# Performance work log

Measured on AMD Instinct MI355X. Metric: run time of the kernel, lower is better.

## Reference

```python
import jax, jax.numpy as jnp
import numpy as np

B = 1024
N_NODES = 30
E_PER = 82
IN_F = 128
HID = 256
HEADS = (3, 2, 1)
N_EH = 41


def _lin(k, fi, fo):
    s = 1.0 / np.sqrt(fi)
    kw, kb = jax.random.split(k)
    W = jax.random.uniform(kw, (fi, fo), jnp.float32, -s, s)
    b = jax.random.uniform(kb, (fo,), jnp.float32, -s, s)
    return W, b


def setup_inputs() -> dict:
    key = jax.random.key(0)
    ks = list(jax.random.split(key, 32))
    rng = np.random.default_rng(0)
    # base 30-node graph with E_PER directed edges, no self-loops
    src = rng.integers(0, N_NODES, E_PER)
    dst = (src + rng.integers(1, N_NODES, E_PER)) % N_NODES
    base = np.stack([src, dst])  # [2, E_PER]
    offs = (np.arange(B) * N_NODES)[None, None, :]  # [1,1,B]
    ei = (base[:, :, None] + offs).transpose(0, 2, 1).reshape(2, -1)  # [2, B*E_PER]
    e_h = rng.choice(E_PER, N_EH, replace=False)
    d = {}
    d["x"] = jax.random.normal(ks[0], (B * N_NODES, IN_F), jnp.float32)
    d["edge_index"] = jnp.asarray(ei, dtype=jnp.int32)
    d["e_h_pairs"] = jnp.asarray(base[:, e_h].T, dtype=jnp.int32)  # [N_EH, 2]
    d["Wp"], d["bp"] = _lin(ks[1], IN_F, HID)
    i = 2
    for l, H in enumerate(HEADS):
        d[f"ln_g{l}"] = jnp.ones((HID,), jnp.float32)
        d[f"ln_b{l}"] = jnp.zeros((HID,), jnp.float32)
        d[f"Wl{l}"], d[f"bl{l}"] = _lin(ks[i], HID, H * HID); i += 1
        d[f"Wr{l}"], d[f"br{l}"] = _lin(ks[i], HID, H * HID); i += 1
        d[f"att{l}"] = jax.random.normal(ks[i], (H, HID), jnp.float32) * 0.1; i += 1
        d[f"bias{l}"] = jnp.zeros((HID,), jnp.float32)
    dims = [2 * HID, 256, 128, 128, 1]
    for j in range(4):
        d[f"Wm{j}"], d[f"bm{j}"] = _lin(ks[i], dims[j], dims[j + 1]); i += 1
    return d


def _layer_norm(h, g, b):
    mu = jnp.mean(h, -1, keepdims=True)
    var = jnp.mean((h - mu) ** 2, -1, keepdims=True)
    return (h - mu) * jax.lax.rsqrt(var + 1e-5) * g + b


def _gatv2(h, src, dst, n, Wl, bl, Wr, br, att, bias):
    # PyG GATv2Conv, concat=False (mean over heads), self-loops already in src/dst
    H, C = att.shape
    xl = (h @ Wl + bl).reshape(-1, H, C)  # source transform
    xr = (h @ Wr + br).reshape(-1, H, C)  # target transform
    xj = xl[src]                          # [E,H,C]
    e = jax.nn.leaky_relu(xj + xr[dst], 0.2)
    logits = jnp.einsum('ehc,hc->eh', e, att)  # [E,H]
    m = jax.lax.stop_gradient(jax.ops.segment_max(logits, dst, num_segments=n))
    ex = jnp.exp(logits - m[dst])
    denom = jax.ops.segment_sum(ex, dst, num_segments=n)
    alpha = ex / denom[dst]               # softmax over incoming edges of dst
    out = jax.ops.segment_sum(xj * alpha[..., None], dst, num_segments=n)  # [N,H,C]
    return jnp.mean(out, 1) + bias


def reference(x, edge_index, e_h_pairs, Wp, bp,
              ln_g0, ln_b0, Wl0, bl0, Wr0, br0, att0, bias0,
              ln_g1, ln_b1, Wl1, bl1, Wr1, br1, att1, bias1,
              ln_g2, ln_b2, Wl2, bl2, Wr2, br2, att2, bias2,
              Wm0, bm0, Wm1, bm1, Wm2, bm2, Wm3, bm3):
    n = x.shape[0]
    loops = jnp.arange(n, dtype=edge_index.dtype)
    src = jnp.concatenate([edge_index[0], loops])
    dst = jnp.concatenate([edge_index[1], loops])
    lrelu = lambda v: jax.nn.leaky_relu(v, 0.01)
    h = x @ Wp + bp
    layers = [(ln_g0, ln_b0, Wl0, bl0, Wr0, br0, att0, bias0),
              (ln_g1, ln_b1, Wl1, bl1, Wr1, br1, att1, bias1),
              (ln_g2, ln_b2, Wl2, bl2, Wr2, br2, att2, bias2)]
    for (g, b, Wl, bl, Wr, br, att, bias) in layers:
        hn = _layer_norm(h, g, b)
        hc = _gatv2(hn, src, dst, n, Wl, bl, Wr, br, att, bias)
        h = lrelu(hc) + h  # dropout is identity in eval
    hb = h.reshape(-1, N_NODES, HID)  # [B, 30, 256]
    ef = jnp.concatenate([hb[:, e_h_pairs[:, 0], :], hb[:, e_h_pairs[:, 1], :]], -1)
    o = ef.reshape(-1, 2 * HID)
    o = lrelu(o @ Wm0 + bm0)
    o = lrelu(o @ Wm1 + bm1)
    o = lrelu(o @ Wm2 + bm2)
    o = o @ Wm3 + bm3
    return o.reshape(-1)
```

## Files before the change

### kernel.cpp

```cpp
#include <hip/hip_runtime.h>
#include <hip/hip_bf16.h>
#include <math.h>

#define N_NODES 30
#define E_BASE  82
#define E_TOT   112
#define B_GRAPH 1024
#define HID     256
#define NTOT    (B_GRAPH * N_NODES)
#define MAXIN   32
#define N_EH    41
#define M_MLP   (B_GRAPH * N_EH)

#define META_SRC  0
#define META_DST  E_TOT
#define META_CNT  (2 * E_TOT)
#define META_LIST 256
#define META_INTS 1216

typedef __attribute__((ext_vector_type(8))) short bf16x8;
typedef __attribute__((ext_vector_type(4))) short bf16x4;
typedef __attribute__((ext_vector_type(4))) float f32x4;
#define AS3 __attribute__((address_space(3)))
#define AS1 __attribute__((address_space(1)))

__device__ __forceinline__ void gload_lds16(const void* g, void* l) {
  __builtin_amdgcn_global_load_lds((const AS1 void*)g, (AS3 void*)l, 16, 0, 0);
}

__device__ __forceinline__ float b2f(short s) {
  union { unsigned u; float f; } x;
  x.u = ((unsigned)(unsigned short)s) << 16;
  return x.f;
}

__global__ void build_graph(const int* __restrict__ ei, int* __restrict__ meta) {
  __shared__ int cnt[N_NODES];
  int tid = threadIdx.x;
  if (tid < N_NODES) cnt[tid] = 0;
  __syncthreads();
  if (tid < E_TOT) {
    int s, d;
    if (tid < E_BASE) { s = ei[tid]; d = ei[B_GRAPH * E_BASE + tid]; }
    else              { s = tid - E_BASE; d = s; }
    meta[META_SRC + tid] = s;
    meta[META_DST + tid] = d;
    int pos = atomicAdd(&cnt[d], 1);
    if (pos < MAXIN) meta[META_LIST + d * MAXIN + pos] = tid;
  }
  __syncthreads();
  if (tid < N_NODES) meta[META_CNT + tid] = cnt[tid];
}

struct WtJob { const float* in; int K, N, tstart, ooff; };
struct WtArgs { WtJob j[10]; };

__global__ __launch_bounds__(256)
void transpose_weights(WtArgs args, __hip_bfloat16* __restrict__ out) {
  int b = blockIdx.x;
  int ji = 0;
  #pragma unroll
  for (int i = 1; i < 10; i++) if (b >= args.j[i].tstart) ji = i;
  WtJob jb = args.j[ji];
  int t = b - jb.tstart;
  int ntn = jb.N >> 5;
  int tk = t / ntn, tn = t - tk * ntn;
  int k0 = tk * 32, n0 = tn * 32;
  __shared__ float s[32][33];
  int tx = threadIdx.x & 31, ty = threadIdx.x >> 5;
  #pragma unroll
  for (int p = 0; p < 4; p++)
    s[ty + p * 8][tx] = jb.in[(size_t)(k0 + ty + p * 8) * jb.N + n0 + tx];
  __syncthreads();
  __hip_bfloat16* o = out + jb.ooff;
  #pragma unroll
  for (int p = 0; p < 4; p++) {
    int n = ty + p * 8;
    o[(size_t)(n0 + n) * jb.K + k0 + tx] = __float2bfloat16(s[tx][n]);
  }
}

__global__ __launch_bounds__(256)
void cast_bf16(const float* __restrict__ in, __hip_bfloat16* __restrict__ out, int n8) {
  int i = blockIdx.x * 256 + threadIdx.x;
  if (i >= n8) return;
  float4 v0 = ((const float4*)in)[i * 2];
  float4 v1 = ((const float4*)in)[i * 2 + 1];
  __hip_bfloat16 t[8];
  t[0] = __float2bfloat16(v0.x); t[1] = __float2bfloat16(v0.y);
  t[2] = __float2bfloat16(v0.z); t[3] = __float2bfloat16(v0.w);
  t[4] = __float2bfloat16(v1.x); t[5] = __float2bfloat16(v1.y);
  t[6] = __float2bfloat16(v1.z); t[7] = __float2bfloat16(v1.w);
  *(bf16x8*)&out[(size_t)i * 8] = *(bf16x8*)t;
}

template<int ACT, int OUTBF>
__global__ __launch_bounds__(256)
void gemm_mfma(const __hip_bfloat16* __restrict__ A, const __hip_bfloat16* __restrict__ Bt,
               const float* __restrict__ bias, const float* __restrict__ bias2,
               void* __restrict__ Cv, int M, int K, int N, int N1)
{
  __shared__ __hip_bfloat16 sA[128 * 32];
  __shared__ __hip_bfloat16 sB[128 * 32];
  const int tid = threadIdx.x;
  const int lane = tid & 63;
  const int wave = tid >> 6;
  const int wx = wave & 1, wy = wave >> 1;
  const int bm = blockIdx.x, bn = blockIdx.y;
  const int mrow = lane & 15, quad = lane >> 4;

  const int r0 = tid >> 2, kc0 = (tid & 3) * 8;
  const __hip_bfloat16* Ag0 = A + (size_t)(bm * 128 + r0) * K + kc0;
  const __hip_bfloat16* Ag1 = A + (size_t)(bm * 128 + r0 + 64) * K + kc0;
  const __hip_bfloat16* Bg0 = Bt + (size_t)(bn * 128 + r0) * K + kc0;
  const __hip_bfloat16* Bg1 = Bt + (size_t)(bn * 128 + r0 + 64) * K + kc0;

  f32x4 acc[4][4];
  #pragma unroll
  for (int i = 0; i < 4; i++)
    #pragma unroll
    for (int j = 0; j < 4; j++)
      acc[i][j] = (f32x4){0.f, 0.f, 0.f, 0.f};

  for (int kt = 0; kt < K; kt += 32) {
    __syncthreads();
    gload_lds16(Ag0 + kt, &sA[tid * 8]);
    gload_lds16(Ag1 + kt, &sA[2048 + tid * 8]);
    gload_lds16(Bg0 + kt, &sB[tid * 8]);
    gload_lds16(Bg1 + kt, &sB[2048 + tid * 8]);
    __syncthreads();

    bf16x8 af[4], bfr[4];
    #pragma unroll
    for (int i = 0; i < 4; i++) {
      af[i]  = *(const bf16x8*)&sA[(wy * 64 + i * 16 + mrow) * 32 + quad * 8];
      bfr[i] = *(const bf16x8*)&sB[(wx * 64 + i * 16 + mrow) * 32 + quad * 8];
    }
    #pragma unroll
    for (int i = 0; i < 4; i++)
      #pragma unroll
      for (int j = 0; j < 4; j++)
        acc[i][j] = __builtin_amdgcn_mfma_f32_16x16x32_bf16(af[i], bfr[j], acc[i][j], 0, 0, 0);
  }

  #pragma unroll
  for (int i = 0; i < 4; i++) {
    #pragma unroll
    for (int r = 0; r < 4; r++) {
      size_t row = (size_t)bm * 128 + wy * 64 + i * 16 + quad * 4 + r;
      #pragma unroll
      for (int j = 0; j < 4; j++) {
        int col = bn * 128 + wx * 64 + j * 16 + mrow;
        float bc = (col < N1) ? bias[col] : bias2[col - N1];
        float v = acc[i][j][r] + bc;
        if (ACT) v = v > 0.f ? v : 0.01f * v;
        if (OUTBF) ((__hip_bfloat16*)Cv)[row * N + col] = __float2bfloat16(v);
        else       ((float*)Cv)[row * N + col] = v;
      }
    }
  }
}

__global__ __launch_bounds__(256)
void gemm_mfma_pair(const float* __restrict__ h, const int* __restrict__ pairs,
                    const __hip_bfloat16* __restrict__ Bt, const float* __restrict__ bias,
                    __hip_bfloat16* __restrict__ C, int N)
{
  const int K = 512;
  __shared__ __hip_bfloat16 sA[128 * 32];
  __shared__ __hip_bfloat16 sB[128 * 32];
  const int tid = threadIdx.x;
  const int lane = tid & 63;
  const int wave = tid >> 6;
  const int wx = wave & 1, wy = wave >> 1;
  const int bm = blockIdx.x, bn = blockIdx.y;
  const int mrow = lane & 15, quad = lane >> 4;

  const float* pu[2]; const float* pv[2]; int sub[2];
  #pragma unroll
  for (int cI = 0; cI < 2; cI++) {
    int c = tid + cI * 256;
    int r0 = c >> 2; sub[cI] = (c & 3) * 8;
    int R = bm * 128 + r0;
    int b = R / N_EH, p = R - b * N_EH;
    int u = pairs[p * 2], v = pairs[p * 2 + 1];
    pu[cI] = h + ((size_t)b * N_NODES + u) * HID;
    pv[cI] = h + ((size_t)b * N_NODES + v) * HID;
  }

  const int r0 = tid >> 2, kc0 = (tid & 3) * 8;
  const __hip_bfloat16* Bg0 = Bt + (size_t)(bn * 128 + r0) * K + kc0;
  const __hip_bfloat16* Bg1 = Bt + (size_t)(bn * 128 + r0 + 64) * K + kc0;

  f32x4 acc[4][4];
  #pragma unroll
  for (int i = 0; i < 4; i++)
    #pragma unroll
    for (int j = 0; j < 4; j++)
      acc[i][j] = (f32x4){0.f, 0.f, 0.f, 0.f};

  for (int kt = 0; kt < K; kt += 32) {
    float4 av[2][2];
    #pragma unroll
    for (int cI = 0; cI < 2; cI++) {
      const float* src = (kt < 256 ? pu[cI] + kt : pv[cI] + kt - 256) + sub[cI];
      av[cI][0] = *(const float4*)src;
      av[cI][1] = *(const float4*)(src + 4);
    }
    __syncthreads();
    #pragma unroll
    for (int cI = 0; cI < 2; cI++) {
      __hip_bfloat16 t[8];
      t[0] = __float2bfloat16(av[cI][0].x); t[1] = __float2bfloat16(av[cI][0].y);
      t[2] = __float2bfloat16(av[cI][0].z); t[3] = __float2bfloat16(av[cI][0].w);
      t[4] = __float2bfloat16(av[cI][1].x); t[5] = __float2bfloat16(av[cI][1].y);
      t[6] = __float2bfloat16(av[cI][1].z); t[7] = __float2bfloat16(av[cI][1].w);
      *(bf16x8*)&sA[(tid + cI * 256) * 8] = *(bf16x8*)t;
    }
    gload_lds16(Bg0 + kt, &sB[tid * 8]);
    gload_lds16(Bg1 + kt, &sB[2048 + tid * 8]);
    __syncthreads();

    bf16x8 af[4], bfr[4];
    #pragma unroll
    for (int i = 0; i < 4; i++) {
      af[i]  = *(const bf16x8*)&sA[(wy * 64 + i * 16 + mrow) * 32 + quad * 8];
      bfr[i] = *(const bf16x8*)&sB[(wx * 64 + i * 16 + mrow) * 32 + quad * 8];
    }
    #pragma unroll
    for (int i = 0; i < 4; i++)
      #pragma unroll
      for (int j = 0; j < 4; j++)
        acc[i][j] = __builtin_amdgcn_mfma_f32_16x16x32_bf16(af[i], bfr[j], acc[i][j], 0, 0, 0);
  }

  #pragma unroll
  for (int i = 0; i < 4; i++) {
    #pragma unroll
    for (int r = 0; r < 4; r++) {
      size_t row = (size_t)bm * 128 + wy * 64 + i * 16 + quad * 4 + r;
      #pragma unroll
      for (int j = 0; j < 4; j++) {
        int col = bn * 128 + wx * 64 + j * 16 + mrow;
        float v = acc[i][j][r] + bias[col];
        v = v > 0.f ? v : 0.01f * v;
        C[row * N + col] = __float2bfloat16(v);
      }
    }
  }
}

__global__ __launch_bounds__(256)
void layernorm(const float* __restrict__ h, const float* __restrict__ g,
               const float* __restrict__ b, __hip_bfloat16* __restrict__ hn)
{
  const int wv = threadIdx.x >> 6, lane = threadIdx.x & 63;
  const size_t row = (size_t)blockIdx.x * 4 + wv;
  const float* hr = h + row * HID;
  float v[4];
  float sum = 0.f;
  #pragma unroll
  for (int j = 0; j < 4; j++) { v[j] = hr[lane + 64 * j]; sum += v[j]; }
  #pragma unroll
  for (int off = 32; off; off >>= 1) sum += __shfl_xor(sum, off);
  float mu = sum * (1.f / 256.f);
  float vs = 0.f;
  #pragma unroll
  for (int j = 0; j < 4; j++) { float d = v[j] - mu; vs += d * d; }
  #pragma unroll
  for (int off = 32; off; off >>= 1) vs += __shfl_xor(vs, off);
  float rs = rsqrtf(vs * (1.f / 256.f) + 1e-5f);
  __hip_bfloat16* outr = hn + row * HID;
  #pragma unroll
  for (int j = 0; j < 4; j++) {
    int c = lane + 64 * j;
    outr[c] = __float2bfloat16((v[j] - mu) * rs * g[c] + b[c]);
  }
}

__global__ __launch_bounds__(256)
void gat_alpha(const __hip_bfloat16* __restrict__ xcat,
               const float* __restrict__ att, float* __restrict__ alphaG,
               const int* __restrict__ meta, int H)
{
  __shared__ float slog[E_TOT];
  __shared__ float smax[N_NODES];
  __shared__ float sden[N_NODES];
  __shared__ int ssrc[E_TOT], sdst[E_TOT], scnt[N_NODES], slist[N_NODES * MAXIN];

  const int tid = threadIdx.x;
  const int g = blockIdx.x, hh = blockIdx.y;
  const size_t nodebase = (size_t)g * N_NODES;
  const int S = 2 * H * HID;

  if (tid < E_TOT) { ssrc[tid] = meta[META_SRC + tid]; sdst[tid] = meta[META_DST + tid]; }
  if (tid < N_NODES) { scnt[tid] = meta[META_CNT + tid]; sden[tid] = 0.f; }
  for (int i = tid; i < N_NODES * MAXIN; i += 256) slist[i] = meta[META_LIST + i];

  const int wv = tid >> 6, l32 = tid & 31, esub = (tid >> 5) & 1;
  const int c0 = l32 * 8;
  float attr[8];
  #pragma unroll
  for (int j = 0; j < 8; j++) attr[j] = att[hh * HID + c0 + j];
  __syncthreads();

  #pragma unroll
  for (int pass = 0; pass < 14; pass++) {
    int e = pass * 8 + wv * 2 + esub;
    int s = ssrc[e], d = sdst[e];
    bf16x8 a = *(const bf16x8*)&xcat[(nodebase + s) * S + hh * HID + c0];
    bf16x8 b = *(const bf16x8*)&xcat[(nodebase + d) * S + (H + hh) * HID + c0];
    float sum = 0.f;
    #pragma unroll
    for (int j = 0; j < 8; j++) {
      float v = b2f(a[j]) + b2f(b[j]);
      v = v > 0.f ? v : 0.2f * v;
      sum += v * attr[j];
    }
    #pragma unroll
    for (int off = 16; off; off >>= 1) sum += __shfl_xor(sum, off);
    if (l32 == 0) slog[e] = sum;
  }
  __syncthreads();

  if (tid < N_NODES) {
    int cnt = scnt[tid];
    const int* lst = &slist[tid * MAXIN];
    float m = -1e30f;
    for (int i = 0; i < cnt; i++) m = fmaxf(m, slog[lst[i]]);
    smax[tid] = m;
  }
  __syncthreads();
  if (tid < E_TOT) {
    float ex = expf(slog[tid] - smax[sdst[tid]]);
    slog[tid] = ex;
    atomicAdd(&sden[sdst[tid]], ex);
  }
  __syncthreads();
  if (tid < E_TOT)
    alphaG[((size_t)g * H + hh) * E_TOT + tid] = slog[tid] / sden[sdst[tid]];
}

template<int DO_LN>
__global__ __launch_bounds__(256, 4)
void gat_agg(const __hip_bfloat16* __restrict__ xcat, const float* __restrict__ alphaG,
             const float* __restrict__ bias, float* __restrict__ h,
             const float* __restrict__ lnG, const float* __restrict__ lnB,
             __hip_bfloat16* __restrict__ hn, const int* __restrict__ meta, int H)
{
  __shared__ __hip_bfloat16 sxl[2][N_NODES * HID];
  __shared__ float salpha[2][E_TOT];
  __shared__ int ssrc[E_TOT], scnt[N_NODES], slist[N_NODES * MAXIN];

  const int tid = threadIdx.x;
  const int g = blockIdx.x;
  const size_t nodebase = (size_t)g * N_NODES;
  const int S = 2 * H * HID;
  const int c4 = tid & 63;
  const int ng = tid >> 6;

  if (tid < E_TOT) ssrc[tid] = meta[META_SRC + tid];
  if (tid < N_NODES) scnt[tid] = meta[META_CNT + tid];
  for (int i = tid; i < N_NODES * MAXIN; i += 256) slist[i] = meta[META_LIST + i];

  float4 hres[8];
  #pragma unroll
  for (int ki = 0; ki < 8; ki++) {
    int k = ng + ki * 4;
    if (k < N_NODES) hres[ki] = *(const float4*)&h[(nodebase + k) * HID + c4 * 4];
  }

  {
    int i = tid;
    #pragma unroll
    for (int p = 0; p < 4; p++, i += 256) {
      if (i < N_NODES * HID / 8) {
        int node = i >> 5, c = (i & 31) * 8;
        gload_lds16(&xcat[(nodebase + node) * S + 0 * HID + c], &sxl[0][(size_t)i * 8]);
      }
    }
    if (tid < E_TOT) salpha[0][tid] = alphaG[((size_t)g * H + 0) * E_TOT + tid];
  }

  float acc[8][4];
  #pragma unroll
  for (int ki = 0; ki < 8; ki++)
    #pragma unroll
    for (int j = 0; j < 4; j++) acc[ki][j] = 0.f;

  for (int hh = 0; hh < H; hh++) {
    const int buf = hh & 1;
    __syncthreads();
    if (hh + 1 < H) {
      const int nb = buf ^ 1;
      int i = tid;
      #pragma unroll
      for (int p = 0; p < 4; p++, i += 256) {
        if (i < N_NODES * HID / 8) {
          int node = i >> 5, c = (i & 31) * 8;
          gload_lds16(&xcat[(nodebase + node) * S + (hh + 1) * HID + c], &sxl[nb][(size_t)i * 8]);
        }
      }
      if (tid < E_TOT) salpha[nb][tid] = alphaG[((size_t)g * H + hh + 1) * E_TOT + tid];
    }
    #pragma unroll
    for (int ki = 0; ki < 8; ki++) {
      int k = ng + ki * 4;
      if (k < N_NODES) {
        int cnt = scnt[k];
        const int* lst = &slist[k * MAXIN];
        for (int i = 0; i < cnt; i++) {
          int e = lst[i];
          float al = salpha[buf][e];
          bf16x4 v = *(const bf16x4*)&sxl[buf][ssrc[e] * HID + c4 * 4];
          acc[ki][0] += al * b2f(v[0]);
          acc[ki][1] += al * b2f(v[1]);
          acc[ki][2] += al * b2f(v[2]);
          acc[ki][3] += al * b2f(v[3]);
        }
      }
    }
  }

  const float invH = 1.f / (float)H;
  const float4 bs = *(const float4*)&bias[c4 * 4];
  float4 gv, bv;
  if (DO_LN) {
    gv = *(const float4*)&lnG[c4 * 4];
    bv = *(const float4*)&lnB[c4 * 4];
  }
  #pragma unroll
  for (int ki = 0; ki < 8; ki++) {
    int k = ng + ki * 4;
    if (k < N_NODES) {
      float o0 = acc[ki][0] * invH + bs.x; o0 = o0 > 0.f ? o0 : 0.01f * o0; o0 += hres[ki].x;
      float o1 = acc[ki][1] * invH + bs.y; o1 = o1 > 0.f ? o1 : 0.01f * o1; o1 += hres[ki].y;
      float o2 = acc[ki][2] * invH + bs.z; o2 = o2 > 0.f ? o2 : 0.01f * o2; o2 += hres[ki].z;
      float o3 = acc[ki][3] * invH + bs.w; o3 = o3 > 0.f ? o3 : 0.01f * o3; o3 += hres[ki].w;
      float4 o4 = {o0, o1, o2, o3};
      *(float4*)&h[(nodebase + k) * HID + c4 * 4] = o4;
      if (DO_LN) {
        float sum = o0 + o1 + o2 + o3;
        #pragma unroll
        for (int off = 32; off; off >>= 1) sum += __shfl_xor(sum, off);
        float mu = sum * (1.f / 256.f);
        float d0 = o0 - mu, d1 = o1 - mu, d2 = o2 - mu, d3 = o3 - mu;
        float vs = d0 * d0 + d1 * d1 + d2 * d2 + d3 * d3;
        #pragma unroll
        for (int off = 32; off; off >>= 1) vs += __shfl_xor(vs, off);
        float rs = rsqrtf(vs * (1.f / 256.f) + 1e-5f);
        __hip_bfloat16 t[4];
        t[0] = __float2bfloat16(d0 * rs * gv.x + bv.x);
        t[1] = __float2bfloat16(d1 * rs * gv.y + bv.y);
        t[2] = __float2bfloat16(d2 * rs * gv.z + bv.z);
        t[3] = __float2bfloat16(d3 * rs * gv.w + bv.w);
        *(bf16x4*)&hn[(nodebase + k) * HID + c4 * 4] = *(bf16x4*)t;
      }
    }
  }
}

__global__ __launch_bounds__(256)
void mlp_out(const float* __restrict__ o3, const float* __restrict__ w,
             const float* __restrict__ b3, float* __restrict__ out)
{
  const int wv = threadIdx.x >> 6, lane = threadIdx.x & 63;
  const int row = blockIdx.x * 4 + wv;
  const float* orow = o3 + (size_t)row * 128;
  float s = orow[lane] * w[lane] + orow[lane + 64] * w[lane + 64];
  #pragma unroll
  for (int off = 32; off; off >>= 1) s += __shfl_xor(s, off);
  if (lane == 0) out[row] = s + b3[0];
}

extern "C" void kernel_launch(void* const* d_in, const int* in_sizes, int n_in,
                              void* d_out, int out_size, void* d_ws, size_t ws_size,
                              hipStream_t stream) {
  const float* x     = (const float*)d_in[0];
  const int*   ei    = (const int*)d_in[1];
  const int*   pairs = (const int*)d_in[2];
  const float* bp    = (const float*)d_in[4];
  const float *lng[3], *lnb[3], *bl[3], *br[3], *att[3], *bias[3];
  const float *WlF[3], *WrF[3];
  for (int l = 0; l < 3; l++) {
    int base = 5 + l * 8;
    lng[l]  = (const float*)d_in[base + 0];
    lnb[l]  = (const float*)d_in[base + 1];
    WlF[l]  = (const float*)d_in[base + 2];
    bl[l]   = (const float*)d_in[base + 3];
    WrF[l]  = (const float*)d_in[base + 4];
    br[l]   = (const float*)d_in[base + 5];
    att[l]  = (const float*)d_in[base + 6];
    bias[l] = (const float*)d_in[base + 7];
  }
  const float* WmF[4] = {(const float*)d_in[29], (const float*)d_in[31],
                         (const float*)d_in[33], (const float*)d_in[35]};
  const float* bm[4] = {(const float*)d_in[30], (const float*)d_in[32],
                        (const float*)d_in[34], (const float*)d_in[36]};

  float* ws  = (float*)d_ws;
  float* h   = ws;
  __hip_bfloat16* hnb = (__hip_bfloat16*)(ws + 7864320);
  __hip_bfloat16* xb  = (__hip_bfloat16*)(ws + 9830400);
  __hip_bfloat16* xcat = (__hip_bfloat16*)(ws + 11796480);
  float* alphaG = ws + 35389440;
  __hip_bfloat16* wbuf = (__hip_bfloat16*)(ws + 35733504);
  int*   meta = (int*)(ws + 36233216);
  __hip_bfloat16* o1b = (__hip_bfloat16*)xcat;
  __hip_bfloat16* o2b = (__hip_bfloat16*)(ws + 17170432);
  float* o3 = ws + 23592960;
  float* out = (float*)d_out;

  const int oWp = 0, oWl0 = 32768, oWr0 = 229376, oWl1 = 425984, oWr1 = 557056;
  const int oWl2 = 688128, oWr2 = 753664, oWm0 = 819200, oWm1 = 950272, oWm2 = 983040;

  build_graph<<<1, 128, 0, stream>>>(ei, meta);

  WtArgs wa;
  wa.j[0] = {(const float*)d_in[3], 128, 256,   0, oWp };
  wa.j[1] = {WlF[0],              256, 768,  32, oWl0};
  wa.j[2] = {WrF[0],              256, 768, 224, oWr0};
  wa.j[3] = {WlF[1],              256, 512, 416, oWl1};
  wa.j[4] = {WrF[1],              256, 512, 544, oWr1};
  wa.j[5] = {WlF[2],              256, 256, 672, oWl2};
  wa.j[6] = {WrF[2],              256, 256, 736, oWr2};
  wa.j[7] = {WmF[0],              512, 256, 800, oWm0};
  wa.j[8] = {WmF[1],              256, 128, 928, oWm1};
  wa.j[9] = {WmF[2],              128, 128, 960, oWm2};
  transpose_weights<<<976, 256, 0, stream>>>(wa, wbuf);

  cast_bf16<<<1920, 256, 0, stream>>>(x, xb, NTOT * 128 / 8);

  gemm_mfma<0, 0><<<dim3(NTOT / 128, 2), 256, 0, stream>>>(xb, wbuf + oWp, bp, bp, h,
                                                           NTOT, 128, 256, 256);

  layernorm<<<NTOT / 4, 256, 0, stream>>>(h, lng[0], lnb[0], hnb);

  const int Hs[3] = {3, 2, 1};
  const int oWl[3] = {oWl0, oWl1, oWl2};
  for (int l = 0; l < 3; l++) {
    int N = 2 * Hs[l] * HID;
    gemm_mfma<0, 1><<<dim3(NTOT / 128, N / 128), 256, 0, stream>>>(
        hnb, wbuf + oWl[l], bl[l], br[l], xcat, NTOT, HID, N, N / 2);
    gat_alpha<<<dim3(B_GRAPH, Hs[l]), 256, 0, stream>>>(xcat, att[l], alphaG, meta, Hs[l]);
    if (l < 2)
      gat_agg<1><<<B_GRAPH, 256, 0, stream>>>(xcat, alphaG, bias[l], h,
                                              lng[l + 1], lnb[l + 1], hnb, meta, Hs[l]);
    else
      gat_agg<0><<<B_GRAPH, 256, 0, stream>>>(xcat, alphaG, bias[l], h,
                                              nullptr, nullptr, nullptr, meta, Hs[l]);
  }

  gemm_mfma_pair<<<dim3(M_MLP / 128, 2), 256, 0, stream>>>(h, pairs, wbuf + oWm0, bm[0], o1b, 256);
  gemm_mfma<1, 1><<<dim3(M_MLP / 128, 1), 256, 0, stream>>>(o1b, wbuf + oWm1, bm[1], bm[1], o2b,
                                                            M_MLP, 256, 128, 128);
  gemm_mfma<1, 0><<<dim3(M_MLP / 128, 1), 256, 0, stream>>>(o2b, wbuf + oWm2, bm[2], bm[2], o3,
                                                            M_MLP, 128, 128, 128);
  mlp_out<<<M_MLP / 4, 256, 0, stream>>>(o3, WmF[3], bm[3], out);
}
```

Baseline: 462.8 us.

## Fuse input bf16 cast into first GEMM and vectorize GEMM epilogue stores

Removes the separate cast_bf16 kernel by adding a GEMM variant that loads fp32 activations directly and converts them to bf16 while staging into LDS. It also swaps the MFMA operand order so each lane holds four consecutive output columns, which lets the epilogue issue 4-wide vector stores and vector bias loads instead of scalar ones. This saves one kernel launch and a full round trip of the bf16 copy of x through memory. The cost is that the fp32 A loads now go through registers rather than direct-to-LDS loads.

```diff
diff --git a/kernel.cpp b/kernel.cpp
--- a/kernel.cpp
+++ b/kernel.cpp
@@ -80,18 +80,26 @@
   }
 }
 
-__global__ __launch_bounds__(256)
-void cast_bf16(const float* __restrict__ in, __hip_bfloat16* __restrict__ out, int n8) {
-  int i = blockIdx.x * 256 + threadIdx.x;
-  if (i >= n8) return;
-  float4 v0 = ((const float4*)in)[i * 2];
-  float4 v1 = ((const float4*)in)[i * 2 + 1];
-  __hip_bfloat16 t[8];
-  t[0] = __float2bfloat16(v0.x); t[1] = __float2bfloat16(v0.y);
-  t[2] = __float2bfloat16(v0.z); t[3] = __float2bfloat16(v0.w);
-  t[4] = __float2bfloat16(v1.x); t[5] = __float2bfloat16(v1.y);
-  t[6] = __float2bfloat16(v1.z); t[7] = __float2bfloat16(v1.w);
-  *(bf16x8*)&out[(size_t)i * 8] = *(bf16x8*)t;
+template<int ACT, int OUTBF>
+__device__ __forceinline__ void store4(void* Cv, size_t row, int colbase, int N,
+                                       const f32x4 a, const float* bias,
+                                       const float* bias2, int N1) {
+  const float* bp = (colbase < N1) ? bias + colbase : bias2 + (colbase - N1);
+  float4 bv = *(const float4*)bp;
+  float v0 = a[0] + bv.x, v1 = a[1] + bv.y, v2 = a[2] + bv.z, v3 = a[3] + bv.w;
+  if (ACT) {
+    v0 = v0 > 0.f ? v0 : 0.01f * v0; v1 = v1 > 0.f ? v1 : 0.01f * v1;
+    v2 = v2 > 0.f ? v2 : 0.01f * v2; v3 = v3 > 0.f ? v3 : 0.01f * v3;
+  }
+  if (OUTBF) {
+    union { __hip_bfloat16 t[4]; uint2 u; } P;
+    P.t[0] = __float2bfloat16(v0); P.t[1] = __float2bfloat16(v1);
+    P.t[2] = __float2bfloat16(v2); P.t[3] = __float2bfloat16(v3);
+    *(uint2*)&((__hip_bfloat16*)Cv)[row * N + colbase] = P.u;
+  } else {
+    float4 o = {v0, v1, v2, v3};
+    *(float4*)&((float*)Cv)[row * N + colbase] = o;
+  }
 }
 
 template<int ACT, int OUTBF>
@@ -140,23 +148,91 @@
     for (int i = 0; i < 4; i++)
       #pragma unroll
       for (int j = 0; j < 4; j++)
-        acc[i][j] = __builtin_amdgcn_mfma_f32_16x16x32_bf16(af[i], bfr[j], acc[i][j], 0, 0, 0);
+        acc[i][j] = __builtin_amdgcn_mfma_f32_16x16x32_bf16(bfr[j], af[i], acc[i][j], 0, 0, 0);
   }
 
   #pragma unroll
   for (int i = 0; i < 4; i++) {
-    #pragma unroll
-    for (int r = 0; r < 4; r++) {
-      size_t row = (size_t)bm * 128 + wy * 64 + i * 16 + quad * 4 + r;
+    size_t row = (size_t)bm * 128 + wy * 64 + i * 16 + mrow;
+    #pragma unroll
+    for (int j = 0; j < 4; j++) {
+      int colbase = bn * 128 + wx * 64 + j * 16 + quad * 4;
+      store4<ACT, OUTBF>(Cv, row, colbase, N, acc[i][j], bias, bias2, N1);
+    }
+  }
+}
+
+template<int ACT, int OUTBF>
+__global__ __launch_bounds__(256)
+void gemm_mfma_f32a(const float* __restrict__ A, const __hip_bfloat16* __restrict__ Bt,
+                    const float* __restrict__ bias, void* __restrict__ Cv,
+                    int M, int K, int N)
+{
+  __shared__ __hip_bfloat16 sA[128 * 32];
+  __shared__ __hip_bfloat16 sB[128 * 32];
+  const int tid = threadIdx.x;
+  const int lane = tid & 63;
+  const int wave = tid >> 6;
+  const int wx = wave & 1, wy = wave >> 1;
+  const int bm = blockIdx.x, bn = blockIdx.y;
+  const int mrow = lane & 15, quad = lane >> 4;
+
+  const int r0 = tid >> 2, kc0 = (tid & 3) * 8;
+  const float* Ag0 = A + (size_t)(bm * 128 + r0) * K + kc0;
+  const float* Ag1 = A + (size_t)(bm * 128 + r0 + 64) * K + kc0;
+  const __hip_bfloat16* Bg0 = Bt + (size_t)(bn * 128 + r0) * K + kc0;
+  const __hip_bfloat16* Bg1 = Bt + (size_t)(bn * 128 + r0 + 64) * K + kc0;
+
+  f32x4 acc[4][4];
+  #pragma unroll
+  for (int i = 0; i < 4; i++)
+    #pragma unroll
+    for (int j = 0; j < 4; j++)
+      acc[i][j] = (f32x4){0.f, 0.f, 0.f, 0.f};
+
+  for (int kt = 0; kt < K; kt += 32) {
+    float4 a00 = *(const float4*)(Ag0 + kt);
+    float4 a01 = *(const float4*)(Ag0 + kt + 4);
+    float4 a10 = *(const float4*)(Ag1 + kt);
+    float4 a11 = *(const float4*)(Ag1 + kt + 4);
+    __syncthreads();
+    {
+      __hip_bfloat16 t[8];
+      t[0] = __float2bfloat16(a00.x); t[1] = __float2bfloat16(a00.y);
+      t[2] = __float2bfloat16(a00.z); t[3] = __float2bfloat16(a00.w);
+      t[4] = __float2bfloat16(a01.x); t[5] = __float2bfloat16(a01.y);
+      t[6] = __float2bfloat16(a01.z); t[7] = __float2bfloat16(a01.w);
+      *(bf16x8*)&sA[tid * 8] = *(bf16x8*)t;
+      t[0] = __float2bfloat16(a10.x); t[1] = __float2bfloat16(a10.y);
+      t[2] = __float2bfloat16(a10.z); t[3] = __float2bfloat16(a10.w);
+      t[4] = __float2bfloat16(a11.x); t[5] = __float2bfloat16(a11.y);
+      t[6] = __float2bfloat16(a11.z); t[7] = __float2bfloat16(a11.w);
+      *(bf16x8*)&sA[2048 + tid * 8] = *(bf16x8*)t;
+    }
+    gload_lds16(Bg0 + kt, &sB[tid * 8]);
+    gload_lds16(Bg1 + kt, &sB[2048 + tid * 8]);
+    __syncthreads();
+
+    bf16x8 af[4], bfr[4];
+    #pragma unroll
+    for (int i = 0; i < 4; i++) {
+      af[i]  = *(const bf16x8*)&sA[(wy * 64 + i * 16 + mrow) * 32 + quad * 8];
+      bfr[i] = *(const bf16x8*)&sB[(wx * 64 + i * 16 + mrow) * 32 + quad * 8];
+    }
+    #pragma unroll
+    for (int i = 0; i < 4; i++)
       #pragma unroll
-      for (int j = 0; j < 4; j++) {
-        int col = bn * 128 + wx * 64 + j * 16 + mrow;
-        float bc = (col < N1) ? bias[col] : bias2[col - N1];
-        float v = acc[i][j][r] + bc;
-        if (ACT) v = v > 0.f ? v : 0.01f * v;
-        if (OUTBF) ((__hip_bfloat16*)Cv)[row * N + col] = __float2bfloat16(v);
-        else       ((float*)Cv)[row * N + col] = v;
-      }
+      for (int j = 0; j < 4; j++)
+        acc[i][j] = __builtin_amdgcn_mfma_f32_16x16x32_bf16(bfr[j], af[i], acc[i][j], 0, 0, 0);
+  }
+
+  #pragma unroll
+  for (int i = 0; i < 4; i++) {
+    size_t row = (size_t)bm * 128 + wy * 64 + i * 16 + mrow;
+    #pragma unroll
+    for (int j = 0; j < 4; j++) {
+      int colbase = bn * 128 + wx * 64 + j * 16 + quad * 4;
+      store4<ACT, OUTBF>(Cv, row, colbase, N, acc[i][j], bias, bias, N);
     }
   }
 }
@@ -231,21 +307,16 @@
     for (int i = 0; i < 4; i++)
       #pragma unroll
       for (int j = 0; j < 4; j++)
-        acc[i][j] = __builtin_amdgcn_mfma_f32_16x16x32_bf16(af[i], bfr[j], acc[i][j], 0, 0, 0);
+        acc[i][j] = __builtin_amdgcn_mfma_f32_16x16x32_bf16(bfr[j], af[i], acc[i][j], 0, 0, 0);
   }
 
   #pragma unroll
   for (int i = 0; i < 4; i++) {
-    #pragma unroll
-    for (int r = 0; r < 4; r++) {
-      size_t row = (size_t)bm * 128 + wy * 64 + i * 16 + quad * 4 + r;
-      #pragma unroll
-      for (int j = 0; j < 4; j++) {
-        int col = bn * 128 + wx * 64 + j * 16 + mrow;
-        float v = acc[i][j][r] + bias[col];
-        v = v > 0.f ? v : 0.01f * v;
-        C[row * N + col] = __float2bfloat16(v);
-      }
+    size_t row = (size_t)bm * 128 + wy * 64 + i * 16 + mrow;
+    #pragma unroll
+    for (int j = 0; j < 4; j++) {
+      int colbase = bn * 128 + wx * 64 + j * 16 + quad * 4;
+      store4<1, 1>(C, row, colbase, N, acc[i][j], bias, bias, N);
     }
   }
 }
@@ -501,7 +572,6 @@
   float* ws  = (float*)d_ws;
   float* h   = ws;
   __hip_bfloat16* hnb = (__hip_bfloat16*)(ws + 7864320);
-  __hip_bfloat16* xb  = (__hip_bfloat16*)(ws + 9830400);
   __hip_bfloat16* xcat = (__hip_bfloat16*)(ws + 11796480);
   float* alphaG = ws + 35389440;
   __hip_bfloat16* wbuf = (__hip_bfloat16*)(ws + 35733504);
@@ -529,10 +599,8 @@
   wa.j[9] = {WmF[2],              128, 128, 960, oWm2};
   transpose_weights<<<976, 256, 0, stream>>>(wa, wbuf);
 
-  cast_bf16<<<1920, 256, 0, stream>>>(x, xb, NTOT * 128 / 8);
-
-  gemm_mfma<0, 0><<<dim3(NTOT / 128, 2), 256, 0, stream>>>(xb, wbuf + oWp, bp, bp, h,
-                                                           NTOT, 128, 256, 256);
+  gemm_mfma_f32a<0, 0><<<dim3(NTOT / 128, 2), 256, 0, stream>>>(x, wbuf + oWp, bp, h,
+                                                                NTOT, 128, 256);
 
   layernorm<<<NTOT / 4, 256, 0, stream>>>(h, lng[0], lnb[0], hnb);
 
```

Result: slower. 500.2 us (+8.1%).
